# Kernel optimization log

Measured on AMD Instinct MI355X. Metric: run time of the kernel, lower is better.

## Reference

```python
import jax, jax.numpy as jnp
import numpy as np
import math

DIM = 512
B, T, H, W = 1, 8, 64, 64


def setup_inputs() -> dict:
    key = jax.random.key(0)
    k0, k1, k2 = jax.random.split(key, 3)
    x = jax.random.normal(k0, (B, DIM, T, H, W), dtype=jnp.float32)
    gamma = jnp.ones((DIM,), jnp.float32)                      # RMS_norm gamma (viewed as flat vector)
    w_qkv = jax.random.normal(k1, (3 * DIM, DIM), jnp.float32) * 0.02  # conv1x1 weight (out, in)
    b_qkv = jnp.zeros((3 * DIM,), jnp.float32)
    w_proj = jax.random.normal(k2, (DIM, DIM), jnp.float32) * 0.02     # zero-init in torch; random for a meaningful baseline
    b_proj = jnp.zeros((DIM,), jnp.float32)
    return dict(x=x, gamma=gamma, w_qkv=w_qkv, b_qkv=b_qkv, w_proj=w_proj, b_proj=b_proj)


def reference(x, gamma, w_qkv, b_qkv, w_proj, b_proj):
    b, c, t, h, w = x.shape
    xt = jnp.transpose(x, (0, 2, 3, 4, 1))          # [b, t, h, w, c]
    identity = xt
    y = xt.reshape(b * t, h, w, c)
    # RMS_norm: L2 norm over channels (last dim), clamped, scaled by sqrt(c)*gamma
    norm = jnp.clip(jnp.linalg.norm(y, axis=-1, keepdims=True), 1e-12, None)
    y = y / norm * (c ** 0.5) * gamma
    # 1x1 conv QKV as GEMM over channels
    qkv = jnp.einsum('bhwc,oc->bhwo', y, w_qkv) + b_qkv        # [bt, h, w, 3c]
    qkv = qkv.reshape(b * t, h * w, 1, 3 * c)                  # nh=1 per source rearrange
    q, k, v = jnp.split(qkv, 3, axis=-1)                       # each [bt, hw, 1, c]
    scale = 1.0 / math.sqrt(c)
    # NOTE: hw sits in the batch position (faithful to source); seq len = nh = 1
    attn = jnp.einsum('bsnc,bsmc->bsnm', q, k) * scale         # [bt, hw, 1, 1]
    attn = jax.nn.softmax(attn, axis=-1)                       # trivially 1.0
    o = jnp.einsum('bsnm,bsmc->bsnc', attn, v)                 # == v
    o = o.reshape(b * t, h, w, c)
    o = jnp.einsum('bhwc,oc->bhwo', o, w_proj) + b_proj        # 1x1 proj conv
    o = o.reshape(b, t, h, w, c)
    out = jnp.transpose(o + identity, (0, 4, 1, 2, 3))         # back to [b, c, t, h, w]
    return out
```

## Files before the change

### kernel.cpp

```cpp
#include <hip/hip_runtime.h>

typedef unsigned short ushort_t;
typedef __attribute__((ext_vector_type(8))) short short8;
typedef __attribute__((ext_vector_type(4))) float f32x4;

#define DIMC 512
#define PN   32768
#define SQRTC 22.627416997969522f

__device__ __forceinline__ ushort_t f2bf(float f) {
  unsigned int u = __float_as_uint(f);
  unsigned int r = u + 0x7fffu + ((u >> 16) & 1u);
  return (ushort_t)(r >> 16);
}

__device__ __forceinline__ int kkey(int r) { return (r & 7) ^ ((r >> 2) & 7); }

__device__ __forceinline__ uint4 pack8(float4 a, float4 b) {
  union { ushort_t u[8]; uint4 v; } r;
  r.u[0] = f2bf(a.x); r.u[1] = f2bf(a.y); r.u[2] = f2bf(a.z); r.u[3] = f2bf(a.w);
  r.u[4] = f2bf(b.x); r.u[5] = f2bf(b.y); r.u[6] = f2bf(b.z); r.u[7] = f2bf(b.w);
  return r.v;
}

__global__ __launch_bounds__(256) void k_wgemm(
    const float* __restrict__ wproj,
    const float* __restrict__ wqkv,
    const float* __restrict__ bqkv,
    const float* __restrict__ bproj,
    const float* __restrict__ gamma,
    ushort_t* __restrict__ Mp2,
    float* __restrict__ fb) {
  int bid = blockIdx.x, tid = threadIdx.x;
  if (bid >= 16) {
    int wave = tid >> 6, lane = tid & 63;
    int o = (bid - 16) * 4 + wave;
    float part = 0.f;
#pragma unroll
    for (int i = 0; i < 8; ++i) {
      int k = lane + i * 64;
      part += wproj[o * DIMC + k] * bqkv[1024 + k];
    }
    for (int off = 32; off; off >>= 1) part += __shfl_down(part, off, 64);
    if (lane == 0) fb[o] = part + bproj[o];
    return;
  }

  __shared__ ushort_t As[128 * 64];
  __shared__ ushort_t Bs[128 * 64];
  int c0 = (bid & 3) * 128;
  int o0 = (bid >> 2) * 128;
  int wave = tid >> 6, lane = tid & 63;
  int wo = (wave & 1) * 64, wp = (wave >> 1) * 64;
  int q = lane >> 4, ln = lane & 15;

  f32x4 zero = {0.f, 0.f, 0.f, 0.f};
  f32x4 acc[4][4];
#pragma unroll
  for (int i = 0; i < 4; ++i)
#pragma unroll
    for (int j = 0; j < 4; ++j) acc[i][j] = zero;

  int sr = tid >> 3;
  int sc = tid & 7;
  const float* Ag = wproj + (long)(o0 + sr) * DIMC + sc * 8;
  int kr = tid >> 5;
  int c4 = (tid & 31) * 4;

  for (int kc = 0; kc < DIMC; kc += 64) {
    __syncthreads();
#pragma unroll
    for (int it = 0; it < 4; ++it) {
      int r = sr + it * 32;
      float4 a0 = *(const float4*)(Ag + (long)it * 32 * DIMC + kc);
      float4 a1 = *(const float4*)(Ag + (long)it * 32 * DIMC + kc + 4);
      *(uint4*)(&As[r * 64 + ((sc ^ (r & 7)) * 8)]) = pack8(a0, a1);
    }
#pragma unroll
    for (int ps = 0; ps < 8; ++ps) {
      int k = kc + ps * 8 + kr;
      float4 b = *(const float4*)(wqkv + (long)(1024 + k) * DIMC + c0 + c4);
      char* bsb = (char*)Bs;
      ushort_t e[4] = {f2bf(b.x), f2bf(b.y), f2bf(b.z), f2bf(b.w)};
#pragma unroll
      for (int i = 0; i < 4; ++i) {
        int c = c4 + i;
        *(ushort_t*)(bsb + c * 128 + ((ps ^ kkey(c)) * 16) + kr * 2) = e[i];
      }
    }
    __syncthreads();
#pragma unroll
    for (int ks = 0; ks < 2; ++ks) {
      int cch = ks * 4 + q;
      short8 af[4], bf[4];
#pragma unroll
      for (int mi = 0; mi < 4; ++mi) {
        int row = wo + mi * 16 + ln;
        af[mi] = *(const short8*)(&As[row * 64 + ((cch ^ (row & 7)) * 8)]);
      }
#pragma unroll
      for (int ni = 0; ni < 4; ++ni) {
        int row = wp + ni * 16 + ln;
        bf[ni] = *(const short8*)(&Bs[row * 64 + ((cch ^ kkey(row)) * 8)]);
      }
#pragma unroll
      for (int mi = 0; mi < 4; ++mi)
#pragma unroll
        for (int ni = 0; ni < 4; ++ni)
          acc[mi][ni] = __builtin_amdgcn_mfma_f32_16x16x32_bf16(af[mi], bf[ni], acc[mi][ni], 0, 0, 0);
    }
  }

#pragma unroll
  for (int mi = 0; mi < 4; ++mi) {
    int obase = o0 + wo + mi * 16 + q * 4;
#pragma unroll
    for (int ni = 0; ni < 4; ++ni) {
      int c = c0 + wp + ni * 16 + ln;
      float g = gamma[c];
      int kb2 = c >> 6, ks2 = (c >> 5) & 1, q2 = (c >> 3) & 3, j2 = c & 7;
#pragma unroll
      for (int r = 0; r < 4; ++r) {
        int o = obase + r;
        int w2 = o >> 6, mi2 = (o >> 4) & 3, ln2 = o & 15;
        long idx = (((((long)w2 * 8 + kb2) * 2 + ks2) * 4 + mi2) * 64 + q2 * 16 + ln2) * 8 + j2;
        Mp2[idx] = f2bf(acc[mi][ni][r] * g);
      }
    }
  }
}

__global__ __launch_bounds__(512, 2) void k_fused(
    const float* __restrict__ x,
    const ushort_t* __restrict__ Mp2,
    const float* __restrict__ fb,
    float* __restrict__ out) {
  __shared__ ushort_t xs[8 * 64 * 64];
  __shared__ float red[32 * 65];
  __shared__ float s_sh[64];
  int tid = threadIdx.x;
  long p0 = (long)blockIdx.x * 64;

  int wave = tid >> 6, lane = tid & 63;
  int q = lane >> 4, ln = lane & 15;

  const ushort_t* Aw = Mp2 + (long)wave * 32768 + lane * 8;

  int pl4 = (tid & 15) * 4;
  int kq  = tid >> 4;
  float4 v[16];
#pragma unroll
  for (int sw = 0; sw < 4; ++sw) {
    const float* xp = x + (long)(kq * 4 + sw * 128) * PN + p0 + pl4;
#pragma unroll
    for (int j = 0; j < 4; ++j)
      v[sw * 4 + j] = *(const float4*)(xp + (long)j * PN);
  }

  short8 afb[2][8];
#pragma unroll
  for (int f = 0; f < 8; ++f) afb[0][f] = *(const short8*)(Aw + f * 512);

  float ss0 = 0.f, ss1 = 0.f, ss2 = 0.f, ss3 = 0.f;
#pragma unroll
  for (int sw = 0; sw < 4; ++sw) {
    int k4 = kq * 4 + sw * 128;
    float4 v0 = v[sw * 4 + 0], v1 = v[sw * 4 + 1];
    float4 v2 = v[sw * 4 + 2], v3 = v[sw * 4 + 3];
    ss0 += v0.x * v0.x + v1.x * v1.x + v2.x * v2.x + v3.x * v3.x;
    ss1 += v0.y * v0.y + v1.y * v1.y + v2.y * v2.y + v3.y * v3.y;
    ss2 += v0.z * v0.z + v1.z * v1.z + v2.z * v2.z + v3.z * v3.z;
    ss3 += v0.w * v0.w + v1.w * v1.w + v2.w * v2.w + v3.w * v3.w;
    ushort_t t0[4] = {f2bf(v0.x), f2bf(v1.x), f2bf(v2.x), f2bf(v3.x)};
    ushort_t t1[4] = {f2bf(v0.y), f2bf(v1.y), f2bf(v2.y), f2bf(v3.y)};
    ushort_t t2[4] = {f2bf(v0.z), f2bf(v1.z), f2bf(v2.z), f2bf(v3.z)};
    ushort_t t3[4] = {f2bf(v0.w), f2bf(v1.w), f2bf(v2.w), f2bf(v3.w)};
    char* base = (char*)xs + (k4 >> 6) * 8192;
    int ch  = (k4 >> 3) & 7;
    int sub = (k4 & 7) * 2;
    *(uint2*)(base + (pl4 + 0) * 128 + ((ch ^ kkey(pl4 + 0)) * 16) + sub) = *(const uint2*)t0;
    *(uint2*)(base + (pl4 + 1) * 128 + ((ch ^ kkey(pl4 + 1)) * 16) + sub) = *(const uint2*)t1;
    *(uint2*)(base + (pl4 + 2) * 128 + ((ch ^ kkey(pl4 + 2)) * 16) + sub) = *(const uint2*)t2;
    *(uint2*)(base + (pl4 + 3) * 128 + ((ch ^ kkey(pl4 + 3)) * 16) + sub) = *(const uint2*)t3;
  }
  red[kq * 65 + pl4 + 0] = ss0;
  red[kq * 65 + pl4 + 1] = ss1;
  red[kq * 65 + pl4 + 2] = ss2;
  red[kq * 65 + pl4 + 3] = ss3;
  __syncthreads();

  if (tid < 64) {
    float t = 0.f;
#pragma unroll
    for (int g = 0; g < 32; ++g) t += red[g * 65 + tid];
    s_sh[tid] = SQRTC / fmaxf(sqrtf(t), 1e-12f);
  }

  f32x4 zero = {0.f, 0.f, 0.f, 0.f};
  f32x4 acc[4][4];
#pragma unroll
  for (int i = 0; i < 4; ++i)
#pragma unroll
    for (int j = 0; j < 4; ++j) acc[i][j] = zero;

#pragma unroll
  for (int kb = 0; kb < 8; ++kb) {
    if (kb < 7) {
#pragma unroll
      for (int f = 0; f < 8; ++f)
        afb[(kb + 1) & 1][f] = *(const short8*)(Aw + ((kb + 1) * 8 + f) * 512);
    }
    const char* bbase = (const char*)xs + kb * 8192;
#pragma unroll
    for (int ks = 0; ks < 2; ++ks) {
      int cch = ks * 4 + q;
      short8 bf[4];
#pragma unroll
      for (int ni = 0; ni < 4; ++ni) {
        int row = ni * 16 + ln;
        bf[ni] = *(const short8*)(bbase + row * 128 + ((cch ^ kkey(row)) * 16));
      }
#pragma unroll
      for (int mi = 0; mi < 4; ++mi)
#pragma unroll
        for (int ni = 0; ni < 4; ++ni)
          acc[mi][ni] = __builtin_amdgcn_mfma_f32_16x16x32_bf16(
              afb[kb & 1][ks * 4 + mi], bf[ni], acc[mi][ni], 0, 0, 0);
    }
  }
  __syncthreads();

  int wo = wave * 64;
#pragma unroll
  for (int mi = 0; mi < 4; ++mi) {
    int obase = wo + mi * 16 + q * 4;
#pragma unroll
    for (int ni = 0; ni < 4; ++ni) {
      int plocal = ni * 16 + ln;
      long p = p0 + plocal;
      float sv = s_sh[plocal];
#pragma unroll
      for (int r = 0; r < 4; ++r) {
        int o = obase + r;
        out[(long)o * PN + p] = x[(long)o * PN + p] + fb[o] + sv * acc[mi][ni][r];
      }
    }
  }
}

extern "C" void kernel_launch(void* const* d_in, const int* in_sizes, int n_in,
                              void* d_out, int out_size, void* d_ws, size_t ws_size,
                              hipStream_t stream) {
  const float* x     = (const float*)d_in[0];
  const float* gamma = (const float*)d_in[1];
  const float* wqkv  = (const float*)d_in[2];
  const float* bqkv  = (const float*)d_in[3];
  const float* wproj = (const float*)d_in[4];
  const float* bproj = (const float*)d_in[5];

  char* ws = (char*)d_ws;
  ushort_t* Mp2 = (ushort_t*)(ws);
  float*    fb  = (float*)(ws + 524288);

  k_wgemm<<<dim3(144), dim3(256), 0, stream>>>(wproj, wqkv, bqkv, bproj, gamma, Mp2, fb);
  k_fused<<<dim3(512), dim3(512), 0, stream>>>(x, Mp2, fb, (float*)d_out);
}
```

Before: 171.4 us.

## Stage fused epilogue through LDS, reuse register x, and use nontemporal float4 stores

The epilogue now transposes the MFMA accumulators through a shared-memory tile (aliased over the x staging buffer) in two halves. Each thread can then write coalesced float4 output rows and add the residual from the x values it already holds in registers, instead of re-reading x from global memory with scattered scalar stores. The bias is cached in LDS and the stores are nontemporal. This removes a second full read of x and makes the writes wider, at the cost of larger shared memory (about 80 KB, which may limit the two-blocks-per-CU occupancy) and extra barriers.

```diff
diff --git a/kernel.cpp b/kernel.cpp
--- a/kernel.cpp
+++ b/kernel.cpp
@@ -135,19 +135,24 @@
     const ushort_t* __restrict__ Mp2,
     const float* __restrict__ fb,
     float* __restrict__ out) {
-  __shared__ ushort_t xs[8 * 64 * 64];
-  __shared__ float red[32 * 65];
-  __shared__ float s_sh[64];
+  __shared__ __align__(16) char smem[80256];
+  ushort_t* xs = (ushort_t*)smem;
+  float* ot    = (float*)smem;
+  float* red   = (float*)(smem + 69632);
+  float* s_sh  = (float*)(smem + 77952);
+  float* fb_sh = (float*)(smem + 78208);
   int tid = threadIdx.x;
   long p0 = (long)blockIdx.x * 64;
 
   int wave = tid >> 6, lane = tid & 63;
   int q = lane >> 4, ln = lane & 15;
-
-  const ushort_t* Aw = Mp2 + (long)wave * 32768 + lane * 8;
-
   int pl4 = (tid & 15) * 4;
   int kq  = tid >> 4;
+
+  const ushort_t* Aw = Mp2 + (long)wave * 32768 + lane * 8;
+
+  fb_sh[tid] = fb[tid];
+
   float4 v[16];
 #pragma unroll
   for (int sw = 0; sw < 4; ++sw) {
@@ -214,37 +219,57 @@
 #pragma unroll
     for (int ks = 0; ks < 2; ++ks) {
       int cch = ks * 4 + q;
-      short8 bf[4];
+      short8 bfr[4];
 #pragma unroll
       for (int ni = 0; ni < 4; ++ni) {
         int row = ni * 16 + ln;
-        bf[ni] = *(const short8*)(bbase + row * 128 + ((cch ^ kkey(row)) * 16));
+        bfr[ni] = *(const short8*)(bbase + row * 128 + ((cch ^ kkey(row)) * 16));
       }
 #pragma unroll
       for (int mi = 0; mi < 4; ++mi)
 #pragma unroll
         for (int ni = 0; ni < 4; ++ni)
           acc[mi][ni] = __builtin_amdgcn_mfma_f32_16x16x32_bf16(
-              afb[kb & 1][ks * 4 + mi], bf[ni], acc[mi][ni], 0, 0, 0);
+              afb[kb & 1][ks * 4 + mi], bfr[ni], acc[mi][ni], 0, 0, 0);
     }
   }
   __syncthreads();
 
-  int wo = wave * 64;
-#pragma unroll
-  for (int mi = 0; mi < 4; ++mi) {
-    int obase = wo + mi * 16 + q * 4;
-#pragma unroll
-    for (int ni = 0; ni < 4; ++ni) {
-      int plocal = ni * 16 + ln;
-      long p = p0 + plocal;
-      float sv = s_sh[plocal];
-#pragma unroll
-      for (int r = 0; r < 4; ++r) {
-        int o = obase + r;
-        out[(long)o * PN + p] = x[(long)o * PN + p] + fb[o] + sv * acc[mi][ni][r];
-      }
-    }
+  int ccmy = (kq >> 3) & 1;
+  float s4x = s_sh[pl4 + 0], s4y = s_sh[pl4 + 1];
+  float s4z = s_sh[pl4 + 2], s4w = s_sh[pl4 + 3];
+#pragma unroll
+  for (int cc = 0; cc < 2; ++cc) {
+#pragma unroll
+    for (int mm = 0; mm < 2; ++mm) {
+      int mi = cc * 2 + mm;
+      int rbase = wave * 32 + mm * 16 + q * 4;
+#pragma unroll
+      for (int ni = 0; ni < 4; ++ni)
+#pragma unroll
+        for (int r = 0; r < 4; ++r)
+          ot[(rbase + r) * 68 + ni * 16 + ln] = acc[mi][ni][r];
+    }
+    __syncthreads();
+    if (ccmy == cc) {
+#pragma unroll
+      for (int sw = 0; sw < 4; ++sw)
+#pragma unroll
+        for (int j = 0; j < 4; ++j) {
+          int o = kq * 4 + sw * 128 + j;
+          int r_loc = (o >> 6) * 32 + (o & 31);
+          const float* gp = ot + r_loc * 68 + pl4;
+          float fbv = fb_sh[o];
+          float4 xv = v[sw * 4 + j];
+          f32x4 res;
+          res[0] = xv.x + fbv + s4x * gp[0];
+          res[1] = xv.y + fbv + s4y * gp[1];
+          res[2] = xv.z + fbv + s4z * gp[2];
+          res[3] = xv.w + fbv + s4w * gp[3];
+          __builtin_nontemporal_store(res, (f32x4*)(out + (long)o * PN + p0 + pl4));
+        }
+    }
+    if (cc == 0) __syncthreads();
   }
 }
 
```

Result: faster. 154.5 us (-9.9%).
